# Optimization experiments

Measured on AMD Instinct MI355X. Metric: run time of the kernel, lower is better.

## Reference

```python
import jax, jax.numpy as jnp
import numpy as np

N_NODES = 100_000
N_EDGES = 1_600_000
NODE_FEATURES = 22


def setup_inputs() -> dict:
    key = jax.random.key(0)
    ks = jax.random.split(key, 10)
    s = 0.1
    x = jax.random.normal(ks[0], (N_NODES, NODE_FEATURES), dtype=jnp.float32)
    edge_index = jax.random.randint(ks[1], (2, N_EDGES), 0, N_NODES, dtype=jnp.int64)
    return {
        "x": x,
        "edge_index": edge_index,
        "W_embed": jax.random.normal(ks[2], (NODE_FEATURES, 32), jnp.float32) * s,
        "b_embed": jax.random.normal(ks[3], (32,), jnp.float32) * s,
        "W1": jax.random.normal(ks[4], (32, 32), jnp.float32) * s,
        "b1": jax.random.normal(ks[5], (32,), jnp.float32) * s,
        "W2": jax.random.normal(ks[6], (64, 32), jnp.float32) * s,
        "b2": jax.random.normal(ks[7], (32,), jnp.float32) * s,
        "W_pred": jax.random.normal(ks[8], (64, 1), jnp.float32) * s,
        "b_pred": jax.random.normal(ks[9], (1,), jnp.float32) * s,
    }


def gcn_conv(h, src, dst, deg_inv_sqrt, W, b, num_nodes):
    """PyG GCNConv: h' = scatter_add(norm_ij * (h W)[src] -> dst) + b.
    src/dst already include self-loops; deg_inv_sqrt precomputed on dst."""
    h = h @ W  # [N, out]
    norm = deg_inv_sqrt[src] * deg_inv_sqrt[dst]  # [E]
    msg = h[src] * norm[:, None]  # gather + normalize
    out = jax.ops.segment_sum(msg, dst, num_segments=num_nodes)  # scatter-add
    return out + b


def reference(x, edge_index, W_embed, b_embed, W1, b1, W2, b2, W_pred, b_pred):
    n = x.shape[0]
    loop = jnp.arange(n, dtype=edge_index.dtype)
    src = jnp.concatenate([edge_index[0], loop])  # add self-loops
    dst = jnp.concatenate([edge_index[1], loop])
    deg = jax.ops.segment_sum(jnp.ones_like(src, dtype=x.dtype), dst, num_segments=n)
    deg_inv_sqrt = jnp.where(deg > 0, jax.lax.rsqrt(jnp.maximum(deg, 1.0)), 0.0)

    h = x @ W_embed + b_embed  # MLP_embed
    # dropout is identity at eval time
    h0 = h
    h = gcn_conv(h, src, dst, deg_inv_sqrt, W1, b1, n)
    h = jax.nn.relu(h)
    h = jnp.concatenate([h, h0], axis=1)  # [N, 64]
    h = gcn_conv(h, src, dst, deg_inv_sqrt, W2, b2, n)
    h = jax.nn.relu(h)
    h = jnp.concatenate([h, h0], axis=1)  # [N, 64]
    delta = h @ W_pred + b_pred  # [N, 1]
    out = jax.nn.relu(delta + x[:, 1:2])
    return out
```

## Files before the change

kernel.cpp:

```cpp
#include <hip/hip_runtime.h>
#include <hip/hip_bf16.h>

#define NF 22
#define H  32
#define BSH 8
#define CAP 8192
#define BCHUNK 4096

__device__ __forceinline__ float bflo(unsigned int v) { return __uint_as_float(v << 16); }
__device__ __forceinline__ float bfhi(unsigned int v) { return __uint_as_float(v & 0xffff0000u); }
__device__ __forceinline__ unsigned int packbf2(float a, float b) {
    __hip_bfloat162 p; p.x = __float2bfloat16(a); p.y = __float2bfloat16(b);
    return *(unsigned int*)&p;
}

__global__ void init_cur(int* __restrict__ cursor, int NB) {
    int i = blockIdx.x * blockDim.x + threadIdx.x;
    if (i < NB) cursor[i] = i * CAP;
}

__global__ __launch_bounds__(512) void bin_edges(
    const int* __restrict__ src, const int* __restrict__ dst,
    int* __restrict__ cursor, int* __restrict__ binned, int E, int NB)
{
    __shared__ int vals[BCHUNK];
    __shared__ unsigned short bkts[BCHUNK];
    __shared__ int svals[BCHUNK];
    __shared__ unsigned short sbkt[BCHUNK];
    __shared__ int scnt[512];
    __shared__ int sex[512];
    __shared__ int lcur[512];
    __shared__ int gbase[512];

    int tid = threadIdx.x;
    for (int j = tid; j < NB; j += 512) scnt[j] = 0;
    __syncthreads();

    int e0 = blockIdx.x * BCHUNK;
    int n = min(e0 + BCHUNK, E) - e0;

    for (int i = tid; i < n; i += 512) {
        int d = dst[e0 + i];
        int b = d >> BSH;
        vals[i] = (src[e0 + i] << BSH) | (d & 255);
        bkts[i] = (unsigned short)b;
        atomicAdd(&scnt[b], 1);
    }
    __syncthreads();

    int c = (tid < NB) ? scnt[tid] : 0;
    int acc = c;
    sex[tid] = acc;
    __syncthreads();
    for (int off = 1; off < 512; off <<= 1) {
        int t = (tid >= off) ? sex[tid - off] : 0;
        __syncthreads();
        sex[tid] += t;
        __syncthreads();
    }
    int ex = sex[tid] - acc;
    __syncthreads();
    sex[tid] = ex;
    lcur[tid] = ex;
    if (tid < NB && c) gbase[tid] = atomicAdd(&cursor[tid], c);
    __syncthreads();

    for (int i = tid; i < n; i += 512) {
        int b = bkts[i];
        int p = atomicAdd(&lcur[b], 1);
        svals[p] = vals[i];
        sbkt[p] = (unsigned short)b;
    }
    __syncthreads();

    for (int i = tid; i < n; i += 512) {
        int b = sbkt[i];
        binned[gbase[b] + (i - sex[b])] = svals[i];
    }
}

__global__ __launch_bounds__(1024) void bucket_csr(
    const int* __restrict__ cursor, const int* __restrict__ binned,
    int* __restrict__ rowptr, int* __restrict__ rowcnt, int* __restrict__ sorted_src,
    float* __restrict__ dis, int N)
{
    __shared__ int cnt[256];
    __shared__ int s[256];
    __shared__ int lcur[256];
    int b = blockIdx.x, tid = threadIdx.x;
    int bn = b << BSH;
    if (tid < 256) cnt[tid] = 0;
    __syncthreads();
    int es = b * CAP, ee = cursor[b];
    for (int i = es + tid; i < ee; i += 1024) atomicAdd(&cnt[binned[i] & 255], 1);
    __syncthreads();
    int v = 0;
    if (tid < 256) { v = cnt[tid]; s[tid] = v; }
    __syncthreads();
    for (int off = 1; off < 256; off <<= 1) {
        int t = 0;
        if (tid < 256 && tid >= off) t = s[tid - off];
        __syncthreads();
        if (tid < 256) s[tid] += t;
        __syncthreads();
    }
    if (tid < 256) {
        int ex = s[tid] - v;
        lcur[tid] = ex;
        int n = bn + tid;
        if (n < N) {
            rowptr[n] = es + ex;
            rowcnt[n] = v;
            dis[n] = rsqrtf((float)(v + 1));
        }
    }
    __syncthreads();
    for (int i = es + tid; i < ee; i += 1024) {
        int e = binned[i];
        int p = atomicAdd(&lcur[e & 255], 1);
        sorted_src[es + p] = e >> BSH;
    }
}

__global__ __launch_bounds__(256) void embed_g1(
    const float* __restrict__ x, const float* __restrict__ We,
    const float* __restrict__ be, const float* __restrict__ W1,
    const float* __restrict__ W2, const float* __restrict__ Wp,
    const float* __restrict__ bp, const float* __restrict__ dis,
    __hip_bfloat16* __restrict__ g, __hip_bfloat16* __restrict__ y2,
    float* __restrict__ hp, int N)
{
    __shared__ float sWe[NF * H];
    __shared__ float sW1[H * H];
    __shared__ float sW2b[H * H];
    __shared__ float sbe[H];
    __shared__ float sWpb[H];
    __shared__ float sx[8][NF];
    __shared__ float sh[8][H];

    int tid = threadIdx.x;
    for (int j = tid; j < NF * H; j += 256) sWe[j] = We[j];
    for (int j = tid; j < H * H; j += 256) sW1[j] = W1[j];
    for (int j = tid; j < H * H; j += 256) sW2b[j] = W2[H * H + j];
    if (tid < H) sbe[tid] = be[tid];
    if (tid >= H && tid < 2 * H) sWpb[tid - H] = Wp[tid];

    int grp = tid >> 5, t = tid & 31;
    int ngrp = (N + 7) >> 3;
    for (int nb = blockIdx.x; nb < ngrp; nb += gridDim.x) {
        int node = nb * 8 + grp;
        int nodec = node < N ? node : N - 1;
        __syncthreads();
        if (t < NF) sx[grp][t] = x[(size_t)nodec * NF + t];
        __syncthreads();

        float h = sbe[t];
#pragma unroll
        for (int k = 0; k < NF; k++) h += sx[grp][k] * sWe[k * H + t];
        sh[grp][t] = h;
        __syncthreads();

        float di = dis[nodec];
        float gv = 0.f, yv = 0.f;
#pragma unroll
        for (int k = 0; k < H; k++) {
            float hv = sh[grp][k];
            gv += hv * sW1[k * H + t];
            yv += hv * sW2b[k * H + t];
        }
        gv *= di;

        float pv = h * sWpb[t];
#pragma unroll
        for (int off = 16; off > 0; off >>= 1) pv += __shfl_down(pv, off, 32);

        if (node < N) {
            size_t o = (size_t)node * H + t;
            g[o] = __float2bfloat16(gv);
            y2[o] = __float2bfloat16(yv);
            if (t == 0) hp[node] = pv + bp[0] + sx[grp][1];
        }
    }
}

__global__ __launch_bounds__(256) void agg_mid(
    const int* __restrict__ rowptr, const int* __restrict__ rowcnt,
    const int* __restrict__ sorted_src,
    const __hip_bfloat16* __restrict__ g_in, const __hip_bfloat16* __restrict__ y2,
    const float* __restrict__ dis, const float* __restrict__ W2,
    const float* __restrict__ b1, __hip_bfloat16* __restrict__ g_out, int N)
{
    __shared__ float sW2[H * H];
    __shared__ float srow[32][33];

    int tid = threadIdx.x;
    for (int j = tid; j < H * H; j += 256) sW2[j] = W2[j];

    int grp = tid >> 3, lane = tid & 7;
    int node = blockIdx.x * 32 + grp;
    int nodec = node < N ? node : N - 1;

    const uint2* gv2 = (const uint2*)g_in;
    uint2 sv = gv2[(size_t)nodec * 8 + lane];
    float a0 = bflo(sv.x), a1 = bfhi(sv.x), a2 = bflo(sv.y), a3 = bfhi(sv.y);

    int start = rowptr[nodec];
    int end = start + rowcnt[nodec];
    int i = start;
    for (; i + 7 < end; i += 8) {
        int s0 = sorted_src[i],     s1 = sorted_src[i + 1];
        int s2 = sorted_src[i + 2], s3 = sorted_src[i + 3];
        int s4 = sorted_src[i + 4], s5 = sorted_src[i + 5];
        int s6 = sorted_src[i + 6], s7 = sorted_src[i + 7];
        uint2 v0 = gv2[(size_t)s0 * 8 + lane], v1 = gv2[(size_t)s1 * 8 + lane];
        uint2 v2 = gv2[(size_t)s2 * 8 + lane], v3 = gv2[(size_t)s3 * 8 + lane];
        uint2 v4 = gv2[(size_t)s4 * 8 + lane], v5 = gv2[(size_t)s5 * 8 + lane];
        uint2 v6 = gv2[(size_t)s6 * 8 + lane], v7 = gv2[(size_t)s7 * 8 + lane];
        a0 += bflo(v0.x) + bflo(v1.x) + bflo(v2.x) + bflo(v3.x)
            + bflo(v4.x) + bflo(v5.x) + bflo(v6.x) + bflo(v7.x);
        a1 += bfhi(v0.x) + bfhi(v1.x) + bfhi(v2.x) + bfhi(v3.x)
            + bfhi(v4.x) + bfhi(v5.x) + bfhi(v6.x) + bfhi(v7.x);
        a2 += bflo(v0.y) + bflo(v1.y) + bflo(v2.y) + bflo(v3.y)
            + bflo(v4.y) + bflo(v5.y) + bflo(v6.y) + bflo(v7.y);
        a3 += bfhi(v0.y) + bfhi(v1.y) + bfhi(v2.y) + bfhi(v3.y)
            + bfhi(v4.y) + bfhi(v5.y) + bfhi(v6.y) + bfhi(v7.y);
    }
    for (; i < end; i++) {
        uint2 v = gv2[(size_t)sorted_src[i] * 8 + lane];
        a0 += bflo(v.x); a1 += bfhi(v.x); a2 += bflo(v.y); a3 += bfhi(v.y);
    }

    float di = dis[nodec];
    float4 bb = ((const float4*)b1)[lane];
    srow[grp][4 * lane]     = fmaxf(di * a0 + bb.x, 0.f);
    srow[grp][4 * lane + 1] = fmaxf(di * a1 + bb.y, 0.f);
    srow[grp][4 * lane + 2] = fmaxf(di * a2 + bb.z, 0.f);
    srow[grp][4 * lane + 3] = fmaxf(di * a3 + bb.w, 0.f);
    __syncthreads();

    const float4* sW2v = (const float4*)sW2;
    float o0 = 0.f, o1 = 0.f, o2 = 0.f, o3 = 0.f;
#pragma unroll
    for (int k = 0; k < H; k++) {
        float rv = srow[grp][k];
        float4 w = sW2v[k * 8 + lane];
        o0 += rv * w.x; o1 += rv * w.y; o2 += rv * w.z; o3 += rv * w.w;
    }
    uint2 yv = ((const uint2*)y2)[(size_t)nodec * 8 + lane];
    o0 = di * (o0 + bflo(yv.x));
    o1 = di * (o1 + bfhi(yv.x));
    o2 = di * (o2 + bflo(yv.y));
    o3 = di * (o3 + bfhi(yv.y));

    if (node < N) {
        uint2 p;
        p.x = packbf2(o0, o1);
        p.y = packbf2(o2, o3);
        ((uint2*)g_out)[(size_t)node * 8 + lane] = p;
    }
}

__global__ __launch_bounds__(256) void agg_final(
    const int* __restrict__ rowptr, const int* __restrict__ rowcnt,
    const int* __restrict__ sorted_src,
    const __hip_bfloat16* __restrict__ g_in, const float* __restrict__ hp,
    const float* __restrict__ dis, const float* __restrict__ b2,
    const float* __restrict__ Wp, float* __restrict__ out, int N)
{
    int gid = blockIdx.x * blockDim.x + threadIdx.x;
    int node = gid >> 3;
    if (node >= N) return;
    int lane = gid & 7;

    const uint2* gv2 = (const uint2*)g_in;
    uint2 sv = gv2[(size_t)node * 8 + lane];
    float a0 = bflo(sv.x), a1 = bfhi(sv.x), a2 = bflo(sv.y), a3 = bfhi(sv.y);

    int start = rowptr[node];
    int end = start + rowcnt[node];
    int i = start;
    for (; i + 7 < end; i += 8) {
        int s0 = sorted_src[i],     s1 = sorted_src[i + 1];
        int s2 = sorted_src[i + 2], s3 = sorted_src[i + 3];
        int s4 = sorted_src[i + 4], s5 = sorted_src[i + 5];
        int s6 = sorted_src[i + 6], s7 = sorted_src[i + 7];
        uint2 v0 = gv2[(size_t)s0 * 8 + lane], v1 = gv2[(size_t)s1 * 8 + lane];
        uint2 v2 = gv2[(size_t)s2 * 8 + lane], v3 = gv2[(size_t)s3 * 8 + lane];
        uint2 v4 = gv2[(size_t)s4 * 8 + lane], v5 = gv2[(size_t)s5 * 8 + lane];
        uint2 v6 = gv2[(size_t)s6 * 8 + lane], v7 = gv2[(size_t)s7 * 8 + lane];
        a0 += bflo(v0.x) + bflo(v1.x) + bflo(v2.x) + bflo(v3.x)
            + bflo(v4.x) + bflo(v5.x) + bflo(v6.x) + bflo(v7.x);
        a1 += bfhi(v0.x) + bfhi(v1.x) + bfhi(v2.x) + bfhi(v3.x)
            + bfhi(v4.x) + bfhi(v5.x) + bfhi(v6.x) + bfhi(v7.x);
        a2 += bflo(v0.y) + bflo(v1.y) + bflo(v2.y) + bflo(v3.y)
            + bflo(v4.y) + bflo(v5.y) + bflo(v6.y) + bflo(v7.y);
        a3 += bfhi(v0.y) + bfhi(v1.y) + bfhi(v2.y) + bfhi(v3.y)
            + bfhi(v4.y) + bfhi(v5.y) + bfhi(v6.y) + bfhi(v7.y);
    }
    for (; i < end; i++) {
        uint2 v = gv2[(size_t)sorted_src[i] * 8 + lane];
        a0 += bflo(v.x); a1 += bfhi(v.x); a2 += bflo(v.y); a3 += bfhi(v.y);
    }

    float di = dis[node];
    float4 b2v = ((const float4*)b2)[lane];
    float4 wp  = ((const float4*)Wp)[lane];
    float v = fmaxf(di * a0 + b2v.x, 0.f) * wp.x
            + fmaxf(di * a1 + b2v.y, 0.f) * wp.y
            + fmaxf(di * a2 + b2v.z, 0.f) * wp.z
            + fmaxf(di * a3 + b2v.w, 0.f) * wp.w;
#pragma unroll
    for (int off = 4; off > 0; off >>= 1) v += __shfl_down(v, off, 8);
    if (lane == 0) out[node] = fmaxf(v + hp[node], 0.f);
}

extern "C" void kernel_launch(void* const* d_in, const int* in_sizes, int n_in,
                              void* d_out, int out_size, void* d_ws, size_t ws_size,
                              hipStream_t stream) {
    const float* x  = (const float*)d_in[0];
    const int*   ei = (const int*)d_in[1];
    const float* We = (const float*)d_in[2];
    const float* be = (const float*)d_in[3];
    const float* W1 = (const float*)d_in[4];
    const float* b1 = (const float*)d_in[5];
    const float* W2 = (const float*)d_in[6];
    const float* b2 = (const float*)d_in[7];
    const float* Wp = (const float*)d_in[8];
    const float* bp = (const float*)d_in[9];
    float* out = (float*)d_out;

    const int N = in_sizes[0] / NF;
    const int E = in_sizes[1] / 2;
    const int* src = ei;
    const int* dst = ei + E;
    const int NB = (N + 255) >> BSH;
    const int nchunk = (E + BCHUNK - 1) / BCHUNK;

    size_t Np  = ((size_t)N + 127) & ~(size_t)127;
    size_t NHp = ((size_t)N * H + 127) & ~(size_t)127;
    float* ws  = (float*)d_ws;
    float* dis = ws;
    float* hp  = dis + Np;
    __hip_bfloat16* g1 = (__hip_bfloat16*)(hp + Np);
    __hip_bfloat16* g2 = g1 + NHp;
    __hip_bfloat16* y2 = g2 + NHp;
    int* cursor     = (int*)(y2 + NHp);
    int* rowptr     = cursor + 512;
    int* rowcnt     = rowptr + Np;
    int* binned     = rowcnt + Np;
    int* sorted_src = binned + (size_t)NB * CAP;

    init_cur<<<2, 256, 0, stream>>>(cursor, NB);
    bin_edges<<<nchunk, 512, 0, stream>>>(src, dst, cursor, binned, E, NB);
    bucket_csr<<<NB, 1024, 0, stream>>>(cursor, binned, rowptr, rowcnt, sorted_src, dis, N);

    int ngrp = (N + 7) >> 3;
    int eg = ngrp < 1536 ? ngrp : 1536;
    embed_g1<<<eg, 256, 0, stream>>>(x, We, be, W1, W2, Wp, bp, dis, g1, y2, hp, N);
    agg_mid<<<(N + 31) / 32, 256, 0, stream>>>(rowptr, rowcnt, sorted_src, g1, y2, dis, W2, b1, g2, N);
    agg_final<<<((size_t)N * 8 + 255) / 256, 256, 0, stream>>>(rowptr, rowcnt, sorted_src, g2, hp, dis, b2, Wp, out, N);
}
```

Measured before the change: 196.3 us.

## Split feature gathers into 16-channel planes and separate mid GEMM kernel

Node feature tables g1/g2 are stored as two 16-channel bf16 planes, and each aggregation runs as two passes over the edges, one per plane. The aim is to keep each gathered plane (about 3.2MB) cache-resident during random gathers. The dense W2 transform moves out of the aggregation into its own mid_gemm kernel, with an intermediate r1 buffer, and the final layer accumulates a partial dot product across the two passes. bucket_csr also stages binned edges in shared memory so global memory is read once instead of twice. The cost is twice the edge-index traffic, more kernel launches and an extra intermediate round trip.

```diff
diff --git a/kernel.cpp b/kernel.cpp
--- a/kernel.cpp
+++ b/kernel.cpp
@@ -84,6 +84,7 @@
     int* __restrict__ rowptr, int* __restrict__ rowcnt, int* __restrict__ sorted_src,
     float* __restrict__ dis, int N)
 {
+    __shared__ int sbin[CAP];
     __shared__ int cnt[256];
     __shared__ int s[256];
     __shared__ int lcur[256];
@@ -92,7 +93,12 @@
     if (tid < 256) cnt[tid] = 0;
     __syncthreads();
     int es = b * CAP, ee = cursor[b];
-    for (int i = es + tid; i < ee; i += 1024) atomicAdd(&cnt[binned[i] & 255], 1);
+    int n = ee - es;
+    for (int i = tid; i < n; i += 1024) {
+        int e = binned[es + i];
+        sbin[i] = e;
+        atomicAdd(&cnt[e & 255], 1);
+    }
     __syncthreads();
     int v = 0;
     if (tid < 256) { v = cnt[tid]; s[tid] = v; }
@@ -107,16 +113,16 @@
     if (tid < 256) {
         int ex = s[tid] - v;
         lcur[tid] = ex;
-        int n = bn + tid;
-        if (n < N) {
-            rowptr[n] = es + ex;
-            rowcnt[n] = v;
-            dis[n] = rsqrtf((float)(v + 1));
+        int nn = bn + tid;
+        if (nn < N) {
+            rowptr[nn] = es + ex;
+            rowcnt[nn] = v;
+            dis[nn] = rsqrtf((float)(v + 1));
         }
     }
     __syncthreads();
-    for (int i = es + tid; i < ee; i += 1024) {
-        int e = binned[i];
+    for (int i = tid; i < n; i += 1024) {
+        int e = sbin[i];
         int p = atomicAdd(&lcur[e & 255], 1);
         sorted_src[es + p] = e >> BSH;
     }
@@ -127,8 +133,8 @@
     const float* __restrict__ be, const float* __restrict__ W1,
     const float* __restrict__ W2, const float* __restrict__ Wp,
     const float* __restrict__ bp, const float* __restrict__ dis,
-    __hip_bfloat16* __restrict__ g, __hip_bfloat16* __restrict__ y2,
-    float* __restrict__ hp, int N)
+    __hip_bfloat16* __restrict__ g1, size_t PSp,
+    __hip_bfloat16* __restrict__ y2, float* __restrict__ hp, int N)
 {
     __shared__ float sWe[NF * H];
     __shared__ float sW1[H * H];
@@ -175,47 +181,40 @@
         for (int off = 16; off > 0; off >>= 1) pv += __shfl_down(pv, off, 32);
 
         if (node < N) {
-            size_t o = (size_t)node * H + t;
-            g[o] = __float2bfloat16(gv);
-            y2[o] = __float2bfloat16(yv);
+            g1[(size_t)(t >> 4) * PSp + (size_t)node * 16 + (t & 15)] = __float2bfloat16(gv);
+            y2[(size_t)node * H + t] = __float2bfloat16(yv);
             if (t == 0) hp[node] = pv + bp[0] + sx[grp][1];
         }
     }
 }
 
-__global__ __launch_bounds__(256) void agg_mid(
+__global__ __launch_bounds__(256) void agg_mid_plane(
     const int* __restrict__ rowptr, const int* __restrict__ rowcnt,
     const int* __restrict__ sorted_src,
-    const __hip_bfloat16* __restrict__ g_in, const __hip_bfloat16* __restrict__ y2,
-    const float* __restrict__ dis, const float* __restrict__ W2,
-    const float* __restrict__ b1, __hip_bfloat16* __restrict__ g_out, int N)
-{
-    __shared__ float sW2[H * H];
-    __shared__ float srow[32][33];
-
-    int tid = threadIdx.x;
-    for (int j = tid; j < H * H; j += 256) sW2[j] = W2[j];
-
-    int grp = tid >> 3, lane = tid & 7;
-    int node = blockIdx.x * 32 + grp;
-    int nodec = node < N ? node : N - 1;
-
-    const uint2* gv2 = (const uint2*)g_in;
-    uint2 sv = gv2[(size_t)nodec * 8 + lane];
+    const __hip_bfloat16* __restrict__ gplane, const float* __restrict__ dis,
+    const float* __restrict__ b1half, unsigned int* __restrict__ r1half, int N)
+{
+    int gid = blockIdx.x * blockDim.x + threadIdx.x;
+    int node = gid >> 2;
+    if (node >= N) return;
+    int lane = gid & 3;
+
+    const uint2* gv2 = (const uint2*)gplane;
+    uint2 sv = gv2[(size_t)node * 4 + lane];
     float a0 = bflo(sv.x), a1 = bfhi(sv.x), a2 = bflo(sv.y), a3 = bfhi(sv.y);
 
-    int start = rowptr[nodec];
-    int end = start + rowcnt[nodec];
+    int start = rowptr[node];
+    int end = start + rowcnt[node];
     int i = start;
     for (; i + 7 < end; i += 8) {
         int s0 = sorted_src[i],     s1 = sorted_src[i + 1];
         int s2 = sorted_src[i + 2], s3 = sorted_src[i + 3];
         int s4 = sorted_src[i + 4], s5 = sorted_src[i + 5];
         int s6 = sorted_src[i + 6], s7 = sorted_src[i + 7];
-        uint2 v0 = gv2[(size_t)s0 * 8 + lane], v1 = gv2[(size_t)s1 * 8 + lane];
-        uint2 v2 = gv2[(size_t)s2 * 8 + lane], v3 = gv2[(size_t)s3 * 8 + lane];
-        uint2 v4 = gv2[(size_t)s4 * 8 + lane], v5 = gv2[(size_t)s5 * 8 + lane];
-        uint2 v6 = gv2[(size_t)s6 * 8 + lane], v7 = gv2[(size_t)s7 * 8 + lane];
+        uint2 v0 = gv2[(size_t)s0 * 4 + lane], v1 = gv2[(size_t)s1 * 4 + lane];
+        uint2 v2 = gv2[(size_t)s2 * 4 + lane], v3 = gv2[(size_t)s3 * 4 + lane];
+        uint2 v4 = gv2[(size_t)s4 * 4 + lane], v5 = gv2[(size_t)s5 * 4 + lane];
+        uint2 v6 = gv2[(size_t)s6 * 4 + lane], v7 = gv2[(size_t)s7 * 4 + lane];
         a0 += bflo(v0.x) + bflo(v1.x) + bflo(v2.x) + bflo(v3.x)
             + bflo(v4.x) + bflo(v5.x) + bflo(v6.x) + bflo(v7.x);
         a1 += bfhi(v0.x) + bfhi(v1.x) + bfhi(v2.x) + bfhi(v3.x)
@@ -226,54 +225,70 @@
             + bfhi(v4.y) + bfhi(v5.y) + bfhi(v6.y) + bfhi(v7.y);
     }
     for (; i < end; i++) {
-        uint2 v = gv2[(size_t)sorted_src[i] * 8 + lane];
+        uint2 v = gv2[(size_t)sorted_src[i] * 4 + lane];
         a0 += bflo(v.x); a1 += bfhi(v.x); a2 += bflo(v.y); a3 += bfhi(v.y);
     }
 
-    float di = dis[nodec];
-    float4 bb = ((const float4*)b1)[lane];
-    srow[grp][4 * lane]     = fmaxf(di * a0 + bb.x, 0.f);
-    srow[grp][4 * lane + 1] = fmaxf(di * a1 + bb.y, 0.f);
-    srow[grp][4 * lane + 2] = fmaxf(di * a2 + bb.z, 0.f);
-    srow[grp][4 * lane + 3] = fmaxf(di * a3 + bb.w, 0.f);
-    __syncthreads();
-
-    const float4* sW2v = (const float4*)sW2;
-    float o0 = 0.f, o1 = 0.f, o2 = 0.f, o3 = 0.f;
+    float di = dis[node];
+    float4 bb = ((const float4*)b1half)[lane];
+    float r0 = fmaxf(di * a0 + bb.x, 0.f);
+    float r1 = fmaxf(di * a1 + bb.y, 0.f);
+    float r2 = fmaxf(di * a2 + bb.z, 0.f);
+    float r3 = fmaxf(di * a3 + bb.w, 0.f);
+    uint2 p;
+    p.x = packbf2(r0, r1);
+    p.y = packbf2(r2, r3);
+    *(uint2*)(r1half + (size_t)node * 16 + lane * 2) = p;
+}
+
+__global__ __launch_bounds__(256) void mid_gemm(
+    const unsigned short* __restrict__ r1, const __hip_bfloat16* __restrict__ y2,
+    const float* __restrict__ dis, const float* __restrict__ W2,
+    __hip_bfloat16* __restrict__ g2, size_t PSp, int N)
+{
+    __shared__ float sW2[H * H];
+    __shared__ float srow[8][33];
+
+    int tid = threadIdx.x;
+    for (int j = tid; j < H * H; j += 256) sW2[j] = W2[j];
+
+    int grp = tid >> 5, t = tid & 31;
+    int ngrp = (N + 7) >> 3;
+    for (int nb = blockIdx.x; nb < ngrp; nb += gridDim.x) {
+        int node = nb * 8 + grp;
+        int nodec = node < N ? node : N - 1;
+        __syncthreads();
+        unsigned short rv = r1[(size_t)nodec * H + t];
+        srow[grp][t] = __uint_as_float((unsigned int)rv << 16);
+        __syncthreads();
+
+        float o = 0.f;
 #pragma unroll
-    for (int k = 0; k < H; k++) {
-        float rv = srow[grp][k];
-        float4 w = sW2v[k * 8 + lane];
-        o0 += rv * w.x; o1 += rv * w.y; o2 += rv * w.z; o3 += rv * w.w;
-    }
-    uint2 yv = ((const uint2*)y2)[(size_t)nodec * 8 + lane];
-    o0 = di * (o0 + bflo(yv.x));
-    o1 = di * (o1 + bfhi(yv.x));
-    o2 = di * (o2 + bflo(yv.y));
-    o3 = di * (o3 + bfhi(yv.y));
-
-    if (node < N) {
-        uint2 p;
-        p.x = packbf2(o0, o1);
-        p.y = packbf2(o2, o3);
-        ((uint2*)g_out)[(size_t)node * 8 + lane] = p;
-    }
-}
-
-__global__ __launch_bounds__(256) void agg_final(
+        for (int k = 0; k < H; k++) o += srow[grp][k] * sW2[k * H + t];
+        unsigned short yu = ((const unsigned short*)y2)[(size_t)nodec * H + t];
+        float di = dis[nodec];
+        o = di * (o + __uint_as_float((unsigned int)yu << 16));
+
+        if (node < N)
+            g2[(size_t)(t >> 4) * PSp + (size_t)node * 16 + (t & 15)] = __float2bfloat16(o);
+    }
+}
+
+__global__ __launch_bounds__(256) void agg_fin_plane(
     const int* __restrict__ rowptr, const int* __restrict__ rowcnt,
     const int* __restrict__ sorted_src,
-    const __hip_bfloat16* __restrict__ g_in, const float* __restrict__ hp,
-    const float* __restrict__ dis, const float* __restrict__ b2,
-    const float* __restrict__ Wp, float* __restrict__ out, int N)
+    const __hip_bfloat16* __restrict__ gplane, const float* __restrict__ dis,
+    const float* __restrict__ b2half, const float* __restrict__ Wphalf,
+    float* __restrict__ partial, const float* __restrict__ hp,
+    float* __restrict__ out, int finish, int N)
 {
     int gid = blockIdx.x * blockDim.x + threadIdx.x;
-    int node = gid >> 3;
+    int node = gid >> 2;
     if (node >= N) return;
-    int lane = gid & 7;
-
-    const uint2* gv2 = (const uint2*)g_in;
-    uint2 sv = gv2[(size_t)node * 8 + lane];
+    int lane = gid & 3;
+
+    const uint2* gv2 = (const uint2*)gplane;
+    uint2 sv = gv2[(size_t)node * 4 + lane];
     float a0 = bflo(sv.x), a1 = bfhi(sv.x), a2 = bflo(sv.y), a3 = bfhi(sv.y);
 
     int start = rowptr[node];
@@ -284,10 +299,10 @@
         int s2 = sorted_src[i + 2], s3 = sorted_src[i + 3];
         int s4 = sorted_src[i + 4], s5 = sorted_src[i + 5];
         int s6 = sorted_src[i + 6], s7 = sorted_src[i + 7];
-        uint2 v0 = gv2[(size_t)s0 * 8 + lane], v1 = gv2[(size_t)s1 * 8 + lane];
-        uint2 v2 = gv2[(size_t)s2 * 8 + lane], v3 = gv2[(size_t)s3 * 8 + lane];
-        uint2 v4 = gv2[(size_t)s4 * 8 + lane], v5 = gv2[(size_t)s5 * 8 + lane];
-        uint2 v6 = gv2[(size_t)s6 * 8 + lane], v7 = gv2[(size_t)s7 * 8 + lane];
+        uint2 v0 = gv2[(size_t)s0 * 4 + lane], v1 = gv2[(size_t)s1 * 4 + lane];
+        uint2 v2 = gv2[(size_t)s2 * 4 + lane], v3 = gv2[(size_t)s3 * 4 + lane];
+        uint2 v4 = gv2[(size_t)s4 * 4 + lane], v5 = gv2[(size_t)s5 * 4 + lane];
+        uint2 v6 = gv2[(size_t)s6 * 4 + lane], v7 = gv2[(size_t)s7 * 4 + lane];
         a0 += bflo(v0.x) + bflo(v1.x) + bflo(v2.x) + bflo(v3.x)
             + bflo(v4.x) + bflo(v5.x) + bflo(v6.x) + bflo(v7.x);
         a1 += bfhi(v0.x) + bfhi(v1.x) + bfhi(v2.x) + bfhi(v3.x)
@@ -298,20 +313,23 @@
             + bfhi(v4.y) + bfhi(v5.y) + bfhi(v6.y) + bfhi(v7.y);
     }
     for (; i < end; i++) {
-        uint2 v = gv2[(size_t)sorted_src[i] * 8 + lane];
+        uint2 v = gv2[(size_t)sorted_src[i] * 4 + lane];
         a0 += bflo(v.x); a1 += bfhi(v.x); a2 += bflo(v.y); a3 += bfhi(v.y);
     }
 
     float di = dis[node];
-    float4 b2v = ((const float4*)b2)[lane];
-    float4 wp  = ((const float4*)Wp)[lane];
-    float v = fmaxf(di * a0 + b2v.x, 0.f) * wp.x
-            + fmaxf(di * a1 + b2v.y, 0.f) * wp.y
-            + fmaxf(di * a2 + b2v.z, 0.f) * wp.z
-            + fmaxf(di * a3 + b2v.w, 0.f) * wp.w;
-#pragma unroll
-    for (int off = 4; off > 0; off >>= 1) v += __shfl_down(v, off, 8);
-    if (lane == 0) out[node] = fmaxf(v + hp[node], 0.f);
+    float4 bb = ((const float4*)b2half)[lane];
+    float4 wp = ((const float4*)Wphalf)[lane];
+    float v = fmaxf(di * a0 + bb.x, 0.f) * wp.x
+            + fmaxf(di * a1 + bb.y, 0.f) * wp.y
+            + fmaxf(di * a2 + bb.z, 0.f) * wp.z
+            + fmaxf(di * a3 + bb.w, 0.f) * wp.w;
+    v += __shfl_down(v, 2, 4);
+    v += __shfl_down(v, 1, 4);
+    if (lane == 0) {
+        if (finish) out[node] = fmaxf(v + partial[node] + hp[node], 0.f);
+        else partial[node] = v;
+    }
 }
 
 extern "C" void kernel_launch(void* const* d_in, const int* in_sizes, int n_in,
@@ -338,13 +356,16 @@
 
     size_t Np  = ((size_t)N + 127) & ~(size_t)127;
     size_t NHp = ((size_t)N * H + 127) & ~(size_t)127;
+    size_t PSp = ((size_t)N * 16 + 127) & ~(size_t)127;
     float* ws  = (float*)d_ws;
     float* dis = ws;
     float* hp  = dis + Np;
-    __hip_bfloat16* g1 = (__hip_bfloat16*)(hp + Np);
-    __hip_bfloat16* g2 = g1 + NHp;
-    __hip_bfloat16* y2 = g2 + NHp;
-    int* cursor     = (int*)(y2 + NHp);
+    float* partial = hp + Np;
+    __hip_bfloat16* g1 = (__hip_bfloat16*)(partial + Np);
+    __hip_bfloat16* g2 = g1 + 2 * PSp;
+    __hip_bfloat16* y2 = g2 + 2 * PSp;
+    unsigned int* r1u  = (unsigned int*)(y2 + NHp);
+    int* cursor     = (int*)(r1u + (size_t)N * 16 + 128);
     int* rowptr     = cursor + 512;
     int* rowcnt     = rowptr + Np;
     int* binned     = rowcnt + Np;
@@ -356,7 +377,12 @@
 
     int ngrp = (N + 7) >> 3;
     int eg = ngrp < 1536 ? ngrp : 1536;
-    embed_g1<<<eg, 256, 0, stream>>>(x, We, be, W1, W2, Wp, bp, dis, g1, y2, hp, N);
-    agg_mid<<<(N + 31) / 32, 256, 0, stream>>>(rowptr, rowcnt, sorted_src, g1, y2, dis, W2, b1, g2, N);
-    agg_final<<<((size_t)N * 8 + 255) / 256, 256, 0, stream>>>(rowptr, rowcnt, sorted_src, g2, hp, dis, b2, Wp, out, N);
-}
+    embed_g1<<<eg, 256, 0, stream>>>(x, We, be, W1, W2, Wp, bp, dis, g1, PSp, y2, hp, N);
+
+    int ag = (int)(((size_t)N * 4 + 255) / 256);
+    agg_mid_plane<<<ag, 256, 0, stream>>>(rowptr, rowcnt, sorted_src, g1,        dis, b1,      r1u,     N);
+    agg_mid_plane<<<ag, 256, 0, stream>>>(rowptr, rowcnt, sorted_src, g1 + PSp,  dis, b1 + 16, r1u + 8, N);
+    mid_gemm<<<eg, 256, 0, stream>>>((const unsigned short*)r1u, y2, dis, W2, g2, PSp, N);
+    agg_fin_plane<<<ag, 256, 0, stream>>>(rowptr, rowcnt, sorted_src, g2,       dis, b2,      Wp,      partial, hp, out, 0, N);
+    agg_fin_plane<<<ag, 256, 0, stream>>>(rowptr, rowcnt, sorted_src, g2 + PSp, dis, b2 + 16, Wp + 16, partial, hp, out, 1, N);
+}
```

Measured after the change: 227.9 us. 16.1% more time.

## Shrink edge-binning blocks, cache bucket in LDS, pack rowptr/count into int2

Applied to the files above, without the earlier changes.

The edge-binning kernel now uses 256 threads over 2048-edge chunks, with each thread scanning two bucket counts. The CSR bucket kernel stages its bucket's edges in shared memory, so the second pass re-reads LDS instead of global memory. Row start and count are packed into one int2, so each aggregation kernel needs one load per node instead of two. The smaller chunks mean twice as many global cursor atomics and write fragments per bucket, and the 32KB LDS array in bucket_csr may reduce occupancy.

```diff
diff --git a/kernel.cpp b/kernel.cpp
--- a/kernel.cpp
+++ b/kernel.cpp
@@ -5,7 +5,7 @@
 #define H  32
 #define BSH 8
 #define CAP 8192
-#define BCHUNK 4096
+#define BCHUNK 2048
 
 __device__ __forceinline__ float bflo(unsigned int v) { return __uint_as_float(v << 16); }
 __device__ __forceinline__ float bfhi(unsigned int v) { return __uint_as_float(v & 0xffff0000u); }
@@ -19,7 +19,7 @@
     if (i < NB) cursor[i] = i * CAP;
 }
 
-__global__ __launch_bounds__(512) void bin_edges(
+__global__ __launch_bounds__(256) void bin_edges(
     const int* __restrict__ src, const int* __restrict__ dst,
     int* __restrict__ cursor, int* __restrict__ binned, int E, int NB)
 {
@@ -33,13 +33,13 @@
     __shared__ int gbase[512];
 
     int tid = threadIdx.x;
-    for (int j = tid; j < NB; j += 512) scnt[j] = 0;
+    for (int j = tid; j < 512; j += 256) scnt[j] = 0;
     __syncthreads();
 
     int e0 = blockIdx.x * BCHUNK;
     int n = min(e0 + BCHUNK, E) - e0;
 
-    for (int i = tid; i < n; i += 512) {
+    for (int i = tid; i < n; i += 256) {
         int d = dst[e0 + i];
         int b = d >> BSH;
         vals[i] = (src[e0 + i] << BSH) | (d & 255);
@@ -48,24 +48,27 @@
     }
     __syncthreads();
 
-    int c = (tid < NB) ? scnt[tid] : 0;
-    int acc = c;
-    sex[tid] = acc;
-    __syncthreads();
-    for (int off = 1; off < 512; off <<= 1) {
+    int c0 = scnt[2 * tid], c1 = scnt[2 * tid + 1];
+    int pair = c0 + c1;
+    sex[tid] = pair;
+    __syncthreads();
+    for (int off = 1; off < 256; off <<= 1) {
         int t = (tid >= off) ? sex[tid - off] : 0;
         __syncthreads();
         sex[tid] += t;
         __syncthreads();
     }
-    int ex = sex[tid] - acc;
-    __syncthreads();
-    sex[tid] = ex;
-    lcur[tid] = ex;
-    if (tid < NB && c) gbase[tid] = atomicAdd(&cursor[tid], c);
-    __syncthreads();
-
-    for (int i = tid; i < n; i += 512) {
+    int pex = sex[tid] - pair;
+    __syncthreads();
+    sex[2 * tid] = pex;
+    sex[2 * tid + 1] = pex + c0;
+    lcur[2 * tid] = pex;
+    lcur[2 * tid + 1] = pex + c0;
+    if (2 * tid < NB && c0) gbase[2 * tid] = atomicAdd(&cursor[2 * tid], c0);
+    if (2 * tid + 1 < NB && c1) gbase[2 * tid + 1] = atomicAdd(&cursor[2 * tid + 1], c1);
+    __syncthreads();
+
+    for (int i = tid; i < n; i += 256) {
         int b = bkts[i];
         int p = atomicAdd(&lcur[b], 1);
         svals[p] = vals[i];
@@ -73,7 +76,7 @@
     }
     __syncthreads();
 
-    for (int i = tid; i < n; i += 512) {
+    for (int i = tid; i < n; i += 256) {
         int b = sbkt[i];
         binned[gbase[b] + (i - sex[b])] = svals[i];
     }
@@ -81,9 +84,10 @@
 
 __global__ __launch_bounds__(1024) void bucket_csr(
     const int* __restrict__ cursor, const int* __restrict__ binned,
-    int* __restrict__ rowptr, int* __restrict__ rowcnt, int* __restrict__ sorted_src,
+    int2* __restrict__ row, int* __restrict__ sorted_src,
     float* __restrict__ dis, int N)
 {
+    __shared__ int sbin[CAP];
     __shared__ int cnt[256];
     __shared__ int s[256];
     __shared__ int lcur[256];
@@ -92,7 +96,12 @@
     if (tid < 256) cnt[tid] = 0;
     __syncthreads();
     int es = b * CAP, ee = cursor[b];
-    for (int i = es + tid; i < ee; i += 1024) atomicAdd(&cnt[binned[i] & 255], 1);
+    int n = ee - es;
+    for (int i = tid; i < n; i += 1024) {
+        int e = binned[es + i];
+        sbin[i] = e;
+        atomicAdd(&cnt[e & 255], 1);
+    }
     __syncthreads();
     int v = 0;
     if (tid < 256) { v = cnt[tid]; s[tid] = v; }
@@ -107,16 +116,15 @@
     if (tid < 256) {
         int ex = s[tid] - v;
         lcur[tid] = ex;
-        int n = bn + tid;
-        if (n < N) {
-            rowptr[n] = es + ex;
-            rowcnt[n] = v;
-            dis[n] = rsqrtf((float)(v + 1));
+        int nn = bn + tid;
+        if (nn < N) {
+            row[nn] = make_int2(es + ex, v);
+            dis[nn] = rsqrtf((float)(v + 1));
         }
     }
     __syncthreads();
-    for (int i = es + tid; i < ee; i += 1024) {
-        int e = binned[i];
+    for (int i = tid; i < n; i += 1024) {
+        int e = sbin[i];
         int p = atomicAdd(&lcur[e & 255], 1);
         sorted_src[es + p] = e >> BSH;
     }
@@ -184,8 +192,7 @@
 }
 
 __global__ __launch_bounds__(256) void agg_mid(
-    const int* __restrict__ rowptr, const int* __restrict__ rowcnt,
-    const int* __restrict__ sorted_src,
+    const int2* __restrict__ row, const int* __restrict__ sorted_src,
     const __hip_bfloat16* __restrict__ g_in, const __hip_bfloat16* __restrict__ y2,
     const float* __restrict__ dis, const float* __restrict__ W2,
     const float* __restrict__ b1, __hip_bfloat16* __restrict__ g_out, int N)
@@ -204,8 +211,8 @@
     uint2 sv = gv2[(size_t)nodec * 8 + lane];
     float a0 = bflo(sv.x), a1 = bfhi(sv.x), a2 = bflo(sv.y), a3 = bfhi(sv.y);
 
-    int start = rowptr[nodec];
-    int end = start + rowcnt[nodec];
+    int2 rw = row[nodec];
+    int start = rw.x, end = rw.x + rw.y;
     int i = start;
     for (; i + 7 < end; i += 8) {
         int s0 = sorted_src[i],     s1 = sorted_src[i + 1];
@@ -261,8 +268,7 @@
 }
 
 __global__ __launch_bounds__(256) void agg_final(
-    const int* __restrict__ rowptr, const int* __restrict__ rowcnt,
-    const int* __restrict__ sorted_src,
+    const int2* __restrict__ row, const int* __restrict__ sorted_src,
     const __hip_bfloat16* __restrict__ g_in, const float* __restrict__ hp,
     const float* __restrict__ dis, const float* __restrict__ b2,
     const float* __restrict__ Wp, float* __restrict__ out, int N)
@@ -276,8 +282,8 @@
     uint2 sv = gv2[(size_t)node * 8 + lane];
     float a0 = bflo(sv.x), a1 = bfhi(sv.x), a2 = bflo(sv.y), a3 = bfhi(sv.y);
 
-    int start = rowptr[node];
-    int end = start + rowcnt[node];
+    int2 rw = row[node];
+    int start = rw.x, end = rw.x + rw.y;
     int i = start;
     for (; i + 7 < end; i += 8) {
         int s0 = sorted_src[i],     s1 = sorted_src[i + 1];
@@ -345,18 +351,17 @@
     __hip_bfloat16* g2 = g1 + NHp;
     __hip_bfloat16* y2 = g2 + NHp;
     int* cursor     = (int*)(y2 + NHp);
-    int* rowptr     = cursor + 512;
-    int* rowcnt     = rowptr + Np;
-    int* binned     = rowcnt + Np;
+    int2* row       = (int2*)(cursor + 512);
+    int* binned     = (int*)(row + Np);
     int* sorted_src = binned + (size_t)NB * CAP;
 
     init_cur<<<2, 256, 0, stream>>>(cursor, NB);
-    bin_edges<<<nchunk, 512, 0, stream>>>(src, dst, cursor, binned, E, NB);
-    bucket_csr<<<NB, 1024, 0, stream>>>(cursor, binned, rowptr, rowcnt, sorted_src, dis, N);
+    bin_edges<<<nchunk, 256, 0, stream>>>(src, dst, cursor, binned, E, NB);
+    bucket_csr<<<NB, 1024, 0, stream>>>(cursor, binned, row, sorted_src, dis, N);
 
     int ngrp = (N + 7) >> 3;
     int eg = ngrp < 1536 ? ngrp : 1536;
     embed_g1<<<eg, 256, 0, stream>>>(x, We, be, W1, W2, Wp, bp, dis, g1, y2, hp, N);
-    agg_mid<<<(N + 31) / 32, 256, 0, stream>>>(rowptr, rowcnt, sorted_src, g1, y2, dis, W2, b1, g2, N);
-    agg_final<<<((size_t)N * 8 + 255) / 256, 256, 0, stream>>>(rowptr, rowcnt, sorted_src, g2, hp, dis, b2, Wp, out, N);
-}
+    agg_mid<<<(N + 31) / 32, 256, 0, stream>>>(row, sorted_src, g1, y2, dis, W2, b1, g2, N);
+    agg_final<<<((size_t)N * 8 + 255) / 256, 256, 0, stream>>>(row, sorted_src, g2, hp, dis, b2, Wp, out, N);
+}
```

New measurement: 218.3 us. +11.2%, slower.
